# Kernel optimization log

Hardware: AMD Instinct MI355X
Metric: run time of the kernel (lower is better)

Reference implementation:

```python
import jax, jax.numpy as jnp
import numpy as np

N_NODES = 50000
N_EDGES = 1600000
NUM_REL = 4
IN_F = 256
OUT_F = 128


def setup_inputs() -> dict:
    key = jax.random.key(0)
    k1, k2, k3 = jax.random.split(key, 3)
    X = jax.random.normal(k1, (N_NODES, IN_F), dtype=jnp.float32)
    # Glorot-ish scale for the per-relation GraphConv weights
    W = jax.random.normal(k2, (NUM_REL, IN_F, OUT_F), dtype=jnp.float32) * (1.0 / np.sqrt(IN_F))
    edge_index = jax.random.randint(k3, (NUM_REL, 2, N_EDGES), 0, N_NODES, dtype=jnp.int64 if jax.config.jax_enable_x64 else jnp.int32)
    return {"X": X, "W": W, "edge_index": edge_index}


def _graph_conv(X, Wr, src, dst, n_nodes):
    """DGL GraphConv, norm='both', bias=False, allow_zero_in_degree=True."""
    ones = jnp.ones(src.shape, dtype=X.dtype)
    out_deg = jax.ops.segment_sum(ones, src, num_segments=n_nodes)
    in_deg = jax.ops.segment_sum(ones, dst, num_segments=n_nodes)
    out_norm = jnp.clip(out_deg, 1.0, None) ** -0.5  # [N]
    in_norm = jnp.clip(in_deg, 1.0, None) ** -0.5    # [N]
    # in_feats > out_feats: apply weight first (same math, cheaper messages)
    h = (X * out_norm[:, None]) @ Wr                 # [N, out]
    agg = jax.ops.segment_sum(h[src], dst, num_segments=n_nodes)  # [N, out]
    return agg * in_norm[:, None]


def reference(X, W, edge_index):
    n_nodes = X.shape[0]
    num_rel = W.shape[0]
    Z = jnp.zeros((n_nodes, W.shape[2]), dtype=X.dtype)
    for r in range(num_rel):  # small fixed loop over relations
        Z = Z + _graph_conv(X, W[r], edge_index[r, 0], edge_index[r, 1], n_nodes)
    return Z
```

## Files before the change

kernel.cpp:

```cpp
#include <hip/hip_runtime.h>

#define IN_F 256
#define OUT_F 128
#define NUM_REL 4
#define BN 64
#define PBX 64
#define PT 512

typedef unsigned int u32;
typedef unsigned short u16;
typedef unsigned char u8;

typedef __attribute__((ext_vector_type(8))) short bf16x8;
typedef __attribute__((ext_vector_type(4))) float f32x4;

static __device__ __forceinline__ u16 f32_to_bf16(float f) {
    union { float f; u32 u; } c; c.f = f;
    u32 u = c.u;
    u32 r = (u + 0x7fffu + ((u >> 16) & 1u)) >> 16;
    return (u16)r;
}
static __device__ __forceinline__ float bf16lo(u32 v) {
    union { u32 u; float f; } c; c.u = v << 16; return c.f;
}
static __device__ __forceinline__ float bf16hi(u32 v) {
    union { u32 u; float f; } c; c.u = v & 0xffff0000u; return c.f;
}

__global__ __launch_bounds__(PT) void p1_hist(const int* __restrict__ EI, u32* __restrict__ ghd,
                                              u32* __restrict__ ghs, int E, int NB, int r0) {
    int rr = blockIdx.y, x = blockIdx.x;
    int r = r0 + rr;
    const int* src = EI + (size_t)(2 * r) * E;
    const int* dst = src + E;
    extern __shared__ u32 sh[];
    u32* hd = sh; u32* hs = sh + NB;
    for (int i = threadIdx.x; i < 2 * NB; i += PT) sh[i] = 0;
    __syncthreads();
    int CH = (E + PBX - 1) / PBX;
    int lo = x * CH, hi = min(E, lo + CH);
    for (int e = lo + threadIdx.x; e < hi; e += PT) {
        atomicAdd(&hd[dst[e] >> 6], 1u);
        atomicAdd(&hs[src[e] >> 6], 1u);
    }
    __syncthreads();
    for (int b = threadIdx.x; b < NB; b += PT) {
        ghd[(size_t)(rr * NB + b) * PBX + x] = hd[b];
        ghs[(size_t)(rr * NB + b) * PBX + x] = hs[b];
    }
}

__global__ __launch_bounds__(256) void p2a_scan(u32* __restrict__ ghd, u32* __restrict__ ghs,
                                                u32* __restrict__ bintot, int BINS) {
    int wid = blockIdx.x * 4 + (threadIdx.x >> 6);
    int lane = threadIdx.x & 63;
    if (wid >= 2 * BINS) return;
    u32* g = (wid < BINS) ? ghd : ghs;
    int bin = (wid < BINS) ? wid : wid - BINS;
    u32 c = g[(size_t)bin * PBX + lane];
    u32 xv = c;
    #pragma unroll
    for (int s = 1; s < 64; s <<= 1) {
        u32 y = __shfl_up(xv, s);
        if (lane >= s) xv += y;
    }
    g[(size_t)bin * PBX + lane] = xv - c;
    if (lane == 63) bintot[wid] = xv;
}

__global__ __launch_bounds__(1024) void p2b_scan(const u32* __restrict__ bintot,
                                                 u32* __restrict__ binbase_d,
                                                 u32* __restrict__ binbase_s, int BINS) {
    __shared__ u32 s[1024];
    __shared__ u32 carry;
    int t = threadIdx.x;
    for (int seg = 0; seg < 2; seg++) {
        const u32* in = bintot + (size_t)seg * BINS;
        u32* out = seg ? binbase_s : binbase_d;
        if (t == 0) carry = 0;
        __syncthreads();
        for (int base = 0; base < BINS; base += 1024) {
            int i = base + t;
            u32 v = (i < BINS) ? in[i] : 0;
            s[t] = v;
            __syncthreads();
            for (int off = 1; off < 1024; off <<= 1) {
                u32 x = (t >= off) ? s[t - off] : 0;
                __syncthreads();
                s[t] += x;
                __syncthreads();
            }
            u32 incl = s[t]; u32 c0 = carry;
            if (i < BINS) out[i] = c0 + incl - v;
            __syncthreads();
            if (t == 1023) carry = c0 + incl;
            __syncthreads();
        }
        if (t == 0) out[BINS] = carry;
        __syncthreads();
    }
}

__global__ __launch_bounds__(PT) void p3_scatter(const int* __restrict__ EI,
                                                 const u32* __restrict__ ghd, const u32* __restrict__ ghs,
                                                 const u32* __restrict__ binbase_d, const u32* __restrict__ binbase_s,
                                                 u32* __restrict__ part_dst, u8* __restrict__ part_src,
                                                 int E, int NB, int r0) {
    int rr = blockIdx.y, x = blockIdx.x;
    int r = r0 + rr;
    const int* src = EI + (size_t)(2 * r) * E;
    const int* dst = src + E;
    extern __shared__ u32 sh[];
    u32* base_d = sh; u32* cur_d = sh + NB; u32* base_s = sh + 2 * NB; u32* cur_s = sh + 3 * NB;
    for (int b = threadIdx.x; b < NB; b += PT) {
        int bin = rr * NB + b;
        base_d[b] = binbase_d[bin] + ghd[(size_t)bin * PBX + x];
        base_s[b] = binbase_s[bin] + ghs[(size_t)bin * PBX + x];
        cur_d[b] = 0; cur_s[b] = 0;
    }
    __syncthreads();
    int CH = (E + PBX - 1) / PBX;
    int lo = x * CH, hi = min(E, lo + CH);
    for (int e = lo + threadIdx.x; e < hi; e += PT) {
        int sv = src[e], dv = dst[e];
        int db = dv >> 6, sb = sv >> 6;
        u32 rk = atomicAdd(&cur_d[db], 1u);
        part_dst[base_d[db] + rk] = ((u32)sv << 6) | (u32)(dv & 63);
        u32 rk2 = atomicAdd(&cur_s[sb], 1u);
        part_src[base_s[sb] + rk2] = (u8)(sv & 63);
    }
}

__global__ __launch_bounds__(256) void srccount_kernel(const u8* __restrict__ part_src,
                                                       const u32* __restrict__ binbase_s,
                                                       float* __restrict__ out_norm, int N, int NB) {
    int b = blockIdx.x, rr = blockIdx.y;
    int bin = rr * NB + b;
    __shared__ u32 cnt[BN];
    int t = threadIdx.x;
    if (t < BN) cnt[t] = 0;
    __syncthreads();
    u32 lo = binbase_s[bin], hi = binbase_s[bin + 1];
    for (u32 i = lo + t; i < hi; i += 256) atomicAdd(&cnt[part_src[i]], 1u);
    __syncthreads();
    if (t < BN) {
        int node = b * BN + t;
        if (node < N) out_norm[(size_t)rr * N + node] = rsqrtf((float)max(cnt[t], 1u));
    }
}

__global__ __launch_bounds__(256) void p4_sort(const u32* __restrict__ part_dst,
                                               const u32* __restrict__ binbase_d,
                                               u32* __restrict__ offs, u16* __restrict__ sorted,
                                               int N, int NB, int nrel) {
    int b = blockIdx.x, rr = blockIdx.y;
    int bin = rr * NB + b;
    __shared__ u32 cnt[BN];
    int t = threadIdx.x;
    if (t < BN) cnt[t] = 0;
    __syncthreads();
    u32 lo = binbase_d[bin], hi = binbase_d[bin + 1];
    for (u32 i = lo + t; i < hi; i += 256) atomicAdd(&cnt[part_dst[i] & 63u], 1u);
    __syncthreads();
    if (t < BN) {
        u32 c = cnt[t];
        u32 x = c;
        #pragma unroll
        for (int s = 1; s < 64; s <<= 1) {
            u32 y = __shfl_up(x, s);
            if (t >= s) x += y;
        }
        u32 excl = x - c;
        int node = b * BN + t;
        if (node < N) offs[(size_t)rr * N + node] = lo + excl;
        cnt[t] = excl;
    }
    __syncthreads();
    for (u32 i = lo + t; i < hi; i += 256) {
        u32 p = part_dst[i];
        u32 pos = atomicAdd(&cnt[p & 63u], 1u);
        sorted[lo + pos] = (u16)(p >> 6);
    }
    if (b == 0 && rr == 0 && t == 0)
        offs[(size_t)nrel * N] = binbase_d[(size_t)nrel * NB];
}

__global__ void wt_kernel(const float* __restrict__ W, u16* __restrict__ BImg, int nrel) {
    int idx = blockIdx.x * 256 + threadIdx.x;
    if (idx >= nrel * 4096) return;
    int r = idx >> 12, q = idx & 4095;
    int ng = q >> 9, kg = (q >> 4) & 31, c = q & 15;
    const float* Wr = W + (size_t)r * IN_F * OUT_F;
    u16 o[8];
    #pragma unroll
    for (int j = 0; j < 8; j++)
        o[j] = f32_to_bf16(Wr[(size_t)(8 * kg + j) * OUT_F + 16 * ng + c]);
    *(uint4*)(BImg + (size_t)idx * 8) = *(const uint4*)o;
}

__global__ void xb_kernel(const float* __restrict__ X, u16* __restrict__ Xb, int N, int nchunks) {
    int idx = blockIdx.x * 256 + threadIdx.x;
    if (idx >= nchunks) return;
    int ci = idx & 1023;
    int S = (idx >> 10) & 3;
    int R = idx >> 12;
    int mg = ci >> 7, kgl = (ci >> 4) & 7, rw = ci & 15;
    int row = R * 128 + mg * 16 + rw;
    int k0 = S * 64 + kgl * 8;
    u16 o[8] = {0, 0, 0, 0, 0, 0, 0, 0};
    if (row < N) {
        const float* xp = X + (size_t)row * IN_F + k0;
        float4 v0 = *(const float4*)xp;
        float4 v1 = *(const float4*)(xp + 4);
        o[0] = f32_to_bf16(v0.x); o[1] = f32_to_bf16(v0.y);
        o[2] = f32_to_bf16(v0.z); o[3] = f32_to_bf16(v0.w);
        o[4] = f32_to_bf16(v1.x); o[5] = f32_to_bf16(v1.y);
        o[6] = f32_to_bf16(v1.z); o[7] = f32_to_bf16(v1.w);
    }
    *(uint4*)(Xb + (size_t)idx * 8) = *(const uint4*)o;
}

__global__ __launch_bounds__(256) void gemm_kernel(const u16* __restrict__ Xb,
                                                   const u16* __restrict__ BImg,
                                                   const float* __restrict__ out_norm,
                                                   u16* __restrict__ h, int N, int r0) {
    int rr = blockIdx.y;
    int r = r0 + rr;
    int R = blockIdx.x;
    int row0 = R * 128;
    __shared__ short Alds[8192];
    __shared__ short Blds[32768];
    int t = threadIdx.x;
    int lane = t & 63, w = t >> 6;
    int wm = w >> 1, wn = w & 1;

    const uint4* bsrc = (const uint4*)(BImg + (size_t)r * 32768);
    uint4* bdst = (uint4*)Blds;
    #pragma unroll
    for (int i = 0; i < 16; i++) bdst[i * 256 + t] = bsrc[i * 256 + t];

    f32x4 acc[4][4];
    #pragma unroll
    for (int mi = 0; mi < 4; mi++)
        #pragma unroll
        for (int ni = 0; ni < 4; ni++) acc[mi][ni] = (f32x4){0.f, 0.f, 0.f, 0.f};

    const uint4* xb4 = (const uint4*)Xb + (size_t)R * 4096;
    uint4 areg[4];
    #pragma unroll
    for (int i = 0; i < 4; i++) areg[i] = xb4[i * 256 + t];

    for (int S = 0; S < 4; S++) {
        uint4* adst = (uint4*)Alds;
        #pragma unroll
        for (int i = 0; i < 4; i++) adst[i * 256 + t] = areg[i];
        __syncthreads();
        if (S < 3) {
            #pragma unroll
            for (int i = 0; i < 4; i++) areg[i] = xb4[(size_t)(S + 1) * 1024 + i * 256 + t];
        }
        #pragma unroll
        for (int kf = 0; kf < 2; kf++) {
            bf16x8 a[4], b[4];
            #pragma unroll
            for (int mi = 0; mi < 4; mi++)
                a[mi] = *(const bf16x8*)(Alds + (wm * 4 + mi) * 1024 + kf * 512 + lane * 8);
            #pragma unroll
            for (int ni = 0; ni < 4; ni++)
                b[ni] = *(const bf16x8*)(Blds + (wn * 4 + ni) * 4096 + S * 1024 + kf * 512 + lane * 8);
            #pragma unroll
            for (int mi = 0; mi < 4; mi++)
                #pragma unroll
                for (int ni = 0; ni < 4; ni++)
                    acc[mi][ni] = __builtin_amdgcn_mfma_f32_16x16x32_bf16(a[mi], b[ni], acc[mi][ni], 0, 0, 0);
        }
        __syncthreads();
    }

    const float* nrm = out_norm + (size_t)rr * N;
    u16* hr = h + (size_t)rr * N * OUT_F;
    #pragma unroll
    for (int mi = 0; mi < 4; mi++) {
        #pragma unroll
        for (int rg = 0; rg < 4; rg++) {
            int row = row0 + wm * 64 + mi * 16 + (lane >> 4) * 4 + rg;
            if (row >= N) continue;
            float nv = nrm[row];
            #pragma unroll
            for (int ni = 0; ni < 4; ni++) {
                int col = wn * 64 + ni * 16 + (lane & 15);
                hr[(size_t)row * OUT_F + col] = f32_to_bf16(acc[mi][ni][rg] * nv);
            }
        }
    }
}

__global__ __launch_bounds__(256) void aggregate_kernel(const u16* __restrict__ sorted,
                                                        const u32* __restrict__ offs,
                                                        const u16* __restrict__ h,
                                                        float* __restrict__ Z,
                                                        int N, int nrel, int accflag) {
    int wid = (blockIdx.x * 256 + threadIdx.x) >> 6;
    int lane = threadIdx.x & 63;
    if (wid >= N) return;
    float t0 = 0.f, t1 = 0.f;
    for (int rr = 0; rr < nrel; rr++) {
        u32 bi = offs[(size_t)rr * N + wid];
        u32 ei = offs[(size_t)rr * N + wid + 1];
        const u32* hr = (const u32*)(h + (size_t)rr * N * OUT_F);
        float a0 = 0.f, a1 = 0.f;
        for (u32 i0 = bi; i0 < ei; i0 += 64u) {
            int m = (int)min(64u, ei - i0);
            u32 v = (lane < m) ? (u32)sorted[i0 + lane] : 0u;
            int j = 0;
            for (; j + 8 <= m; j += 8) {
                u32 rg[8];
                #pragma unroll
                for (int q = 0; q < 8; q++)
                    rg[q] = hr[(size_t)__shfl(v, j + q) * (OUT_F / 2) + lane];
                #pragma unroll
                for (int q = 0; q < 8; q++) { a0 += bf16lo(rg[q]); a1 += bf16hi(rg[q]); }
            }
            for (; j < m; j++) {
                u32 rv = hr[(size_t)__shfl(v, j) * (OUT_F / 2) + lane];
                a0 += bf16lo(rv); a1 += bf16hi(rv);
            }
        }
        float inr = rsqrtf((float)max(ei - bi, 1u));
        t0 += inr * a0;
        t1 += inr * a1;
    }
    float2* zp = (float2*)(Z + (size_t)wid * OUT_F + lane * 2);
    if (accflag) { float2 z = *zp; z.x += t0; z.y += t1; *zp = z; }
    else         { *zp = make_float2(t0, t1); }
}

extern "C" void kernel_launch(void* const* d_in, const int* in_sizes, int n_in,
                              void* d_out, int out_size, void* d_ws, size_t ws_size,
                              hipStream_t stream) {
    const float* X = (const float*)d_in[0];
    const float* W = (const float*)d_in[1];
    const int* EI = (const int*)d_in[2];
    float* Z = (float*)d_out;
    const int N = in_sizes[0] / IN_F;
    const int E = in_sizes[2] / (NUM_REL * 2);
    const int NB = (N + BN - 1) / BN;
    const int RBcnt = (N + 127) / 128;

    size_t sorted_o, offs_o, out_norm_o, bbd_o, bbs_o, xb_o, bimg_o, h_o,
           ghd_o, ghs_o, bintot_o, part_dst_o, part_src_o;
    auto layout = [&](int nb) -> size_t {
        size_t cur = 0;
        auto alloc = [&](size_t bytes) {
            size_t o = cur; cur = (cur + bytes + 255) & ~(size_t)255; return o;
        };
        int BINS = nb * NB;
        size_t TE = (size_t)nb * E;
        sorted_o   = alloc(TE * 2);
        offs_o     = alloc(((size_t)nb * N + 1) * 4);
        out_norm_o = alloc((size_t)nb * N * 4);
        bbd_o      = alloc((size_t)(BINS + 1) * 4);
        bbs_o      = alloc((size_t)(BINS + 1) * 4);
        xb_o       = alloc((size_t)RBcnt * 4096 * 16);
        bimg_o     = alloc((size_t)NUM_REL * 4096 * 16);
        h_o        = alloc((size_t)nb * N * OUT_F * 2);
        size_t hend = cur;
        size_t ov = h_o;
        auto oalloc = [&](size_t bytes) {
            size_t o = ov; ov = (ov + bytes + 255) & ~(size_t)255; return o;
        };
        ghd_o      = oalloc((size_t)BINS * PBX * 4);
        ghs_o      = oalloc((size_t)BINS * PBX * 4);
        bintot_o   = oalloc((size_t)2 * BINS * 4);
        part_dst_o = oalloc(TE * 4);
        part_src_o = oalloc(TE);
        return (ov > hend) ? ov : hend;
    };
    int nb = NUM_REL;
    while (nb > 1 && layout(nb) > ws_size) nb >>= 1;
    layout(nb);
    char* ws = (char*)d_ws;
    const int nbatches = (NUM_REL + nb - 1) / nb;

    u16* xb = (u16*)(ws + xb_o);
    u16* bimg = (u16*)(ws + bimg_o);

    int nchunks = RBcnt * 4096;
    xb_kernel<<<(nchunks + 255) / 256, 256, 0, stream>>>(X, xb, N, nchunks);
    wt_kernel<<<(NUM_REL * 4096 + 255) / 256, 256, 0, stream>>>(W, bimg, NUM_REL);

    if (nbatches > 1)
        hipMemsetAsync(d_out, 0, (size_t)N * OUT_F * sizeof(float), stream);

    for (int r0 = 0; r0 < NUM_REL; r0 += nb) {
        int cur = min(nb, NUM_REL - r0);
        int BINS = cur * NB;
        u16* sorted   = (u16*)(ws + sorted_o);
        u32* offs     = (u32*)(ws + offs_o);
        float* out_norm = (float*)(ws + out_norm_o);
        u32* bbd      = (u32*)(ws + bbd_o);
        u32* bbs      = (u32*)(ws + bbs_o);
        u16* h        = (u16*)(ws + h_o);
        u32* ghd      = (u32*)(ws + ghd_o);
        u32* ghs      = (u32*)(ws + ghs_o);
        u32* bintot   = (u32*)(ws + bintot_o);
        u32* part_dst = (u32*)(ws + part_dst_o);
        u8* part_src  = (u8*)(ws + part_src_o);

        p1_hist<<<dim3(PBX, cur), PT, 2 * NB * 4, stream>>>(EI, ghd, ghs, E, NB, r0);
        p2a_scan<<<(2 * BINS + 3) / 4, 256, 0, stream>>>(ghd, ghs, bintot, BINS);
        p2b_scan<<<1, 1024, 0, stream>>>(bintot, bbd, bbs, BINS);
        p3_scatter<<<dim3(PBX, cur), PT, 4 * NB * 4, stream>>>(
            EI, ghd, ghs, bbd, bbs, part_dst, part_src, E, NB, r0);
        srccount_kernel<<<dim3(NB, cur), 256, 0, stream>>>(part_src, bbs, out_norm, N, NB);
        p4_sort<<<dim3(NB, cur), 256, 0, stream>>>(part_dst, bbd, offs, sorted, N, NB, cur);
        gemm_kernel<<<dim3(RBcnt, cur), 256, 0, stream>>>(xb, bimg, out_norm, h, N, r0);
        aggregate_kernel<<<((size_t)N * 64 + 255) / 256, 256, 0, stream>>>(
            sorted, offs, h, Z, N, cur, (nbatches > 1) ? 1 : 0);
    }
}
```

Baseline: 472.5 us.

## Aggregate four destination nodes per wavefront with 16-byte row loads

The aggregation kernel now assigns a 16-lane group to each destination node, so one wavefront handles four nodes. Each lane loads a uint4 (8 bf16 values) per neighbor row instead of one u32, and neighbor ids are read directly from memory rather than broadcast with shuffles. The aim is to cut lane idleness and shuffle overhead for the low-degree nodes here (about 32 edges per relation) and to issue wider memory transactions. The cost is more registers per lane and divergence between groups when node degrees differ.

```diff
diff --git a/kernel.cpp b/kernel.cpp
--- a/kernel.cpp
+++ b/kernel.cpp
@@ -302,37 +302,55 @@
                                                         int N, int nrel, int accflag) {
     int wid = (blockIdx.x * 256 + threadIdx.x) >> 6;
     int lane = threadIdx.x & 63;
-    if (wid >= N) return;
-    float t0 = 0.f, t1 = 0.f;
+    int g = lane >> 4, l16 = lane & 15;
+    int dst = wid * 4 + g;
+    int dstc = (dst < N) ? dst : (N - 1);
+    float t[8] = {0.f, 0.f, 0.f, 0.f, 0.f, 0.f, 0.f, 0.f};
     for (int rr = 0; rr < nrel; rr++) {
-        u32 bi = offs[(size_t)rr * N + wid];
-        u32 ei = offs[(size_t)rr * N + wid + 1];
-        const u32* hr = (const u32*)(h + (size_t)rr * N * OUT_F);
-        float a0 = 0.f, a1 = 0.f;
-        for (u32 i0 = bi; i0 < ei; i0 += 64u) {
-            int m = (int)min(64u, ei - i0);
-            u32 v = (lane < m) ? (u32)sorted[i0 + lane] : 0u;
-            int j = 0;
-            for (; j + 8 <= m; j += 8) {
-                u32 rg[8];
-                #pragma unroll
-                for (int q = 0; q < 8; q++)
-                    rg[q] = hr[(size_t)__shfl(v, j + q) * (OUT_F / 2) + lane];
-                #pragma unroll
-                for (int q = 0; q < 8; q++) { a0 += bf16lo(rg[q]); a1 += bf16hi(rg[q]); }
+        u32 b = offs[(size_t)rr * N + dstc];
+        u32 e = offs[(size_t)rr * N + dstc + 1];
+        u32 cnt = (dst < N) ? (e - b) : 0u;
+        const uint4* hr = (const uint4*)(h + (size_t)rr * N * OUT_F);
+        float a[8] = {0.f, 0.f, 0.f, 0.f, 0.f, 0.f, 0.f, 0.f};
+        u32 j = 0;
+        for (; j + 8 <= cnt; j += 8) {
+            u32 ids[8];
+            #pragma unroll
+            for (int q = 0; q < 8; q++) ids[q] = (u32)sorted[b + j + q];
+            uint4 rv[8];
+            #pragma unroll
+            for (int q = 0; q < 8; q++) rv[q] = hr[(size_t)ids[q] * 16 + l16];
+            #pragma unroll
+            for (int q = 0; q < 8; q++) {
+                a[0] += bf16lo(rv[q].x); a[1] += bf16hi(rv[q].x);
+                a[2] += bf16lo(rv[q].y); a[3] += bf16hi(rv[q].y);
+                a[4] += bf16lo(rv[q].z); a[5] += bf16hi(rv[q].z);
+                a[6] += bf16lo(rv[q].w); a[7] += bf16hi(rv[q].w);
             }
-            for (; j < m; j++) {
-                u32 rv = hr[(size_t)__shfl(v, j) * (OUT_F / 2) + lane];
-                a0 += bf16lo(rv); a1 += bf16hi(rv);
-            }
-        }
-        float inr = rsqrtf((float)max(ei - bi, 1u));
-        t0 += inr * a0;
-        t1 += inr * a1;
-    }
-    float2* zp = (float2*)(Z + (size_t)wid * OUT_F + lane * 2);
-    if (accflag) { float2 z = *zp; z.x += t0; z.y += t1; *zp = z; }
-    else         { *zp = make_float2(t0, t1); }
+        }
+        for (; j < cnt; j++) {
+            uint4 rv = hr[(size_t)sorted[b + j] * 16 + l16];
+            a[0] += bf16lo(rv.x); a[1] += bf16hi(rv.x);
+            a[2] += bf16lo(rv.y); a[3] += bf16hi(rv.y);
+            a[4] += bf16lo(rv.z); a[5] += bf16hi(rv.z);
+            a[6] += bf16lo(rv.w); a[7] += bf16hi(rv.w);
+        }
+        float inr = rsqrtf((float)max(cnt, 1u));
+        #pragma unroll
+        for (int k = 0; k < 8; k++) t[k] += inr * a[k];
+    }
+    if (dst < N) {
+        float4* zp = (float4*)(Z + (size_t)dst * OUT_F + l16 * 8);
+        if (accflag) {
+            float4 z0 = zp[0], z1 = zp[1];
+            z0.x += t[0]; z0.y += t[1]; z0.z += t[2]; z0.w += t[3];
+            z1.x += t[4]; z1.y += t[5]; z1.z += t[6]; z1.w += t[7];
+            zp[0] = z0; zp[1] = z1;
+        } else {
+            zp[0] = make_float4(t[0], t[1], t[2], t[3]);
+            zp[1] = make_float4(t[4], t[5], t[6], t[7]);
+        }
+    }
 }
 
 extern "C" void kernel_launch(void* const* d_in, const int* in_sizes, int n_in,
@@ -415,7 +433,7 @@
         srccount_kernel<<<dim3(NB, cur), 256, 0, stream>>>(part_src, bbs, out_norm, N, NB);
         p4_sort<<<dim3(NB, cur), 256, 0, stream>>>(part_dst, bbd, offs, sorted, N, NB, cur);
         gemm_kernel<<<dim3(RBcnt, cur), 256, 0, stream>>>(xb, bimg, out_norm, h, N, r0);
-        aggregate_kernel<<<((size_t)N * 64 + 255) / 256, 256, 0, stream>>>(
+        aggregate_kernel<<<(N + 15) / 16, 256, 0, stream>>>(
             sorted, offs, h, Z, N, cur, (nbatches > 1) ? 1 : 0);
     }
 }
```

Result: faster. 461.5 us (-2.3%).
